# Kernel tuning notes

Hardware: AMD Instinct MI355X
Metric: run time of the kernel (lower is better)

Reference implementation:

```python
import jax, jax.numpy as jnp
import numpy as np

EPS = 1e-08


def _norm(H, add):
    # Faithful to GTN.norm: transpose, mask/set diagonal, row-normalize by degree, transpose back.
    # The original O(N^3) mm(deg_inv_diag, H) is expressed as an O(N^2) row scaling (same math).
    Ht = H.T
    n = Ht.shape[0]
    eye = jnp.eye(n, dtype=H.dtype)
    Ht = Ht * (1.0 - eye)
    if add:
        Ht = Ht + eye
    deg = jnp.sum(Ht, axis=1)
    deg_inv = jnp.where(deg == 0, 0.0, 1.0 / (deg + EPS))
    return (deg_inv[:, None] * Ht).T


def _gtconv(A, w):
    # A: [E, N, N]; w: [C, E, 1, 1] -> softmax over E, weighted sum of adjacency channels.
    s = jax.nn.softmax(w[:, :, 0, 0], axis=1)  # [C, E]
    return jnp.einsum('ce,eij->cij', s, A)     # [C, N, N]


def setup_inputs() -> dict:
    key = jax.random.key(0)
    k = jax.random.split(key, 6)
    E, N, C, w_in, w_out = 5, 2048, 2, 256, 64
    A = jax.random.uniform(k[0], (E, N, N), dtype=jnp.float32)
    X = jax.random.normal(k[1], (N, w_in), dtype=jnp.float32)
    conv_w_l0_1 = jax.random.normal(k[2], (C, E, 1, 1), dtype=jnp.float32)
    conv_w_l0_2 = jax.random.normal(k[3], (C, E, 1, 1), dtype=jnp.float32)
    conv_w_l1 = jax.random.normal(k[4], (C, E, 1, 1), dtype=jnp.float32)
    gcn_weight = jax.random.normal(k[5], (w_in, w_out), dtype=jnp.float32) * (1.0 / np.sqrt(w_in))
    return {"A": A, "X": X, "conv_w_l0_1": conv_w_l0_1, "conv_w_l0_2": conv_w_l0_2,
            "conv_w_l1": conv_w_l1, "gcn_weight": gcn_weight}


def reference(A, X, conv_w_l0_1, conv_w_l0_2, conv_w_l1, gcn_weight):
    N = A.shape[1]
    # Layer 0 (first=True): two GTConvs, meta-path composition via bmm.
    a = _gtconv(A, conv_w_l0_1)            # [C, N, N]
    b = _gtconv(A, conv_w_l0_2)            # [C, N, N]
    H = jnp.einsum('cij,cjk->cik', a, b)   # [C, N, N]
    # Layer 1 (first=False): normalize per channel, then compose with new conv.
    H = jax.vmap(lambda h: _norm(h, False))(H)
    a1 = _gtconv(A, conv_w_l1)
    H = jnp.einsum('cij,cjk->cik', H, a1)
    # GCN readout per channel: mm(norm_add(H_c).T, X @ W), relu, concat along features.
    Xw = X @ gcn_weight                     # [N, w_out]
    Hn = jax.vmap(lambda h: _norm(h, True))(H)   # [C, N, N]
    Xc = jax.nn.relu(jnp.einsum('cji,jk->cik', Hn, Xw))  # [C, N, w_out]
    X_ = jnp.transpose(Xc, (1, 0, 2)).reshape(N, -1)     # [N, C*w_out]
    return X_
```

## Files before the change

### kernel.cpp

```cpp
#include <hip/hip_runtime.h>
#include <cstdint>
#include <cstddef>

typedef unsigned short u16;
typedef __attribute__((ext_vector_type(8))) short short8;
typedef __attribute__((ext_vector_type(4))) float v4f;

static constexpr size_t NN = (size_t)2048 * 2048;
#define N2 2048

typedef __attribute__((address_space(1))) const unsigned int guint;
typedef __attribute__((address_space(3))) unsigned int luint;

__device__ __forceinline__ float b2f_bits(uint32_t hi) { union { uint32_t u; float f; } v; v.u = hi; return v.f; }
__device__ __forceinline__ float b2f(u16 x) { return b2f_bits((uint32_t)x << 16); }
__device__ __forceinline__ u16 f2b(float f) {
  union { float f; uint32_t u; } v; v.f = f;
  uint32_t r = v.u + 0x7fffu + ((v.u >> 16) & 1u);
  return (u16)(r >> 16);
}
__device__ __forceinline__ uint4 pack8(const float* f) {
  uint4 u;
  u.x = (uint32_t)f2b(f[0]) | ((uint32_t)f2b(f[1]) << 16);
  u.y = (uint32_t)f2b(f[2]) | ((uint32_t)f2b(f[3]) << 16);
  u.z = (uint32_t)f2b(f[4]) | ((uint32_t)f2b(f[5]) << 16);
  u.w = (uint32_t)f2b(f[6]) | ((uint32_t)f2b(f[7]) << 16);
  return u;
}
__device__ __forceinline__ void unp8(uint4 u, float* f) {
  f[0] = b2f_bits(u.x << 16); f[1] = b2f_bits(u.x & 0xffff0000u);
  f[2] = b2f_bits(u.y << 16); f[3] = b2f_bits(u.y & 0xffff0000u);
  f[4] = b2f_bits(u.z << 16); f[5] = b2f_bits(u.z & 0xffff0000u);
  f[6] = b2f_bits(u.w << 16); f[7] = b2f_bits(u.w & 0xffff0000u);
}

__global__ __launch_bounds__(256, 2) void conv_kernel(
    const float* __restrict__ A, const float* __restrict__ w1,
    const float* __restrict__ w2, const float* __restrict__ w3,
    const float* __restrict__ X, const float* __restrict__ W,
    u16* __restrict__ abf, u16* __restrict__ bbt, u16* __restrict__ a1t,
    u16* __restrict__ a1r, u16* __restrict__ Xwt)
{
  __shared__ u16 LT[4][64][72];
  const int t = threadIdx.x;
  const int i0 = blockIdx.y * 64, j0 = blockIdx.x * 64;

  const int row = t >> 2;
  const int cq = (t & 3) * 16;

  float fa[5][16];
  #pragma unroll
  for (int e = 0; e < 5; ++e) {
    const float* base = A + (size_t)e * NN + (size_t)(i0 + row) * N2 + (j0 + cq);
    #pragma unroll
    for (int m = 0; m < 4; ++m) {
      float4 v = *(const float4*)(base + m * 4);
      fa[e][m * 4 + 0] = v.x; fa[e][m * 4 + 1] = v.y;
      fa[e][m * 4 + 2] = v.z; fa[e][m * 4 + 3] = v.w;
    }
  }

  const float* wsrc[3] = { w1, w2, w3 };
  #pragma unroll
  for (int c = 0; c < 2; ++c) {
    float sc[3][5];
    #pragma unroll
    for (int q = 0; q < 3; ++q) {
      float v[5], mx = -1e30f, sum = 0.f;
      #pragma unroll
      for (int e = 0; e < 5; ++e) { v[e] = wsrc[q][c * 5 + e]; mx = fmaxf(mx, v[e]); }
      #pragma unroll
      for (int e = 0; e < 5; ++e) { v[e] = expf(v[e] - mx); sum += v[e]; }
      #pragma unroll
      for (int e = 0; e < 5; ++e) sc[q][e] = v[e] / sum;
    }
    float av[16], bv[16], cv[16];
    #pragma unroll
    for (int u = 0; u < 16; ++u) { av[u] = 0.f; bv[u] = 0.f; cv[u] = 0.f; }
    #pragma unroll
    for (int e = 0; e < 5; ++e)
      #pragma unroll
      for (int u = 0; u < 16; ++u) {
        av[u] += sc[0][e] * fa[e][u];
        bv[u] += sc[1][e] * fa[e][u];
        cv[u] += sc[2][e] * fa[e][u];
      }
    {
      uint4* pa = (uint4*)(abf + (size_t)c * NN + (size_t)(i0 + row) * N2 + (j0 + cq));
      pa[0] = pack8(av); pa[1] = pack8(av + 8);
      uint4* pr = (uint4*)(a1r + (size_t)c * NN + (size_t)(i0 + row) * N2 + (j0 + cq));
      pr[0] = pack8(cv); pr[1] = pack8(cv + 8);
    }
    #pragma unroll
    for (int u = 0; u < 16; ++u) {
      LT[c][cq + u][row]     = f2b(bv[u]);
      LT[2 + c][cq + u][row] = f2b(cv[u]);
    }
  }
  __syncthreads();
  {
    const int on = t >> 2;
    const int om = (t & 3) * 16;
    #pragma unroll
    for (int c = 0; c < 2; ++c) {
      const uint4* pb = (const uint4*)&LT[c][on][om];
      uint4* pd = (uint4*)(bbt + (size_t)c * NN + (size_t)(j0 + on) * N2 + (i0 + om));
      pd[0] = pb[0]; pd[1] = pb[1];
      const uint4* pc = (const uint4*)&LT[2 + c][on][om];
      uint4* pe = (uint4*)(a1t + (size_t)c * NN + (size_t)(j0 + on) * N2 + (i0 + om));
      pe[0] = pc[0]; pe[1] = pc[1];
    }
  }
  if (blockIdx.y < 16) {
    const int n = (int)(blockIdx.y * 32 + blockIdx.x) * 4 + (t >> 6);
    const int k = t & 63;
    float acc = 0.f;
    for (int m = 0; m < 256; ++m)
      acc += X[n * 256 + m] * W[m * 64 + k];
    Xwt[(size_t)k * N2 + n] = f2b(acc);
  }
}

template<bool TOUT>
__global__ __launch_bounds__(256, 3) void gemm_kernel(
    const u16* __restrict__ Ain, const u16* __restrict__ Btin,
    u16* __restrict__ Cout, float* __restrict__ csp, float* __restrict__ diag)
{
  const int c = blockIdx.z;
  const u16* Ac = Ain + (size_t)c * NN;
  const u16* Bc = Btin + (size_t)c * NN;
  const int m0 = blockIdx.y * 128, n0 = blockIdx.x * 128;
  const int t = threadIdx.x, w = t >> 6, lane = t & 63;
  const int quad = lane >> 4, r = lane & 15;
  __shared__ u16 SM[128 * 64 + 128 * 64];
  u16* As = SM;
  u16* Bs = SM + 128 * 64;

  v4f zero4 = { 0.f, 0.f, 0.f, 0.f };
  v4f acc[2][8];
  #pragma unroll
  for (int i = 0; i < 2; ++i)
    #pragma unroll
    for (int j = 0; j < 8; ++j) acc[i][j] = zero4;

  const int srow = lane >> 3;
  const int sgran = (lane & 7) ^ srow;

  for (int kt = 0; kt < 2048; kt += 64) {
    __syncthreads();
    #pragma unroll
    for (int i = 0; i < 4; ++i) {
      const int chunk = i * 4 + w;
      const u16* ga = Ac + (size_t)(m0 + chunk * 8 + srow) * N2 + kt + sgran * 8;
      __builtin_amdgcn_global_load_lds((guint*)ga, (luint*)(As + chunk * 512), 16, 0, 0);
    }
    #pragma unroll
    for (int i = 0; i < 4; ++i) {
      const int chunk = i * 4 + w;
      const u16* gb = Bc + (size_t)(n0 + chunk * 8 + srow) * N2 + kt + sgran * 8;
      __builtin_amdgcn_global_load_lds((guint*)gb, (luint*)(Bs + chunk * 512), 16, 0, 0);
    }
    __syncthreads();
    #pragma unroll
    for (int ks = 0; ks < 2; ++ks) {
      const int sl = ((ks * 4 + quad) ^ (r & 7)) * 8;
      short8 af[2], bf[8];
      #pragma unroll
      for (int i = 0; i < 2; ++i)
        af[i] = *(const short8*)(As + (w * 32 + i * 16 + r) * 64 + sl);
      #pragma unroll
      for (int j = 0; j < 8; ++j)
        bf[j] = *(const short8*)(Bs + (j * 16 + r) * 64 + sl);
      #pragma unroll
      for (int i = 0; i < 2; ++i)
        #pragma unroll
        for (int j = 0; j < 8; ++j)
          acc[i][j] = __builtin_amdgcn_mfma_f32_16x16x32_bf16(af[i], bf[j], acc[i][j], 0, 0, 0);
    }
  }
  if (blockIdx.x == blockIdx.y) {
    #pragma unroll
    for (int i = 0; i < 2; ++i) {
      const int rowg = m0 + w * 32 + i * 16 + quad * 4;
      #pragma unroll
      for (int j = 0; j < 8; ++j) {
        const int colg = n0 + j * 16 + r;
        #pragma unroll
        for (int g = 0; g < 4; ++g)
          if (rowg + g == colg) diag[c * N2 + colg] = acc[i][j][g];
      }
    }
  }
  if constexpr (!TOUT) {
    u16* Cc = Cout + (size_t)c * NN;
    #pragma unroll
    for (int i = 0; i < 2; ++i) {
      const int rowg = m0 + w * 32 + i * 16 + quad * 4;
      #pragma unroll
      for (int j = 0; j < 8; ++j) {
        const int colg = n0 + j * 16 + r;
        #pragma unroll
        for (int g = 0; g < 4; ++g)
          Cc[(size_t)(rowg + g) * N2 + colg] = f2b(acc[i][j][g]);
      }
    }
  }
  float s[8];
  #pragma unroll
  for (int j = 0; j < 8; ++j) {
    s[j] = 0.f;
    #pragma unroll
    for (int i = 0; i < 2; ++i)
      #pragma unroll
      for (int g = 0; g < 4; ++g) s[j] += acc[i][j][g];
    s[j] += __shfl_xor(s[j], 16);
    s[j] += __shfl_xor(s[j], 32);
  }
  __syncthreads();
  float* csl = (float*)SM;
  if (quad == 0) {
    #pragma unroll
    for (int j = 0; j < 8; ++j) csl[w * 128 + j * 16 + r] = s[j];
  }
  __syncthreads();
  if (t < 128) {
    const float v = csl[t] + csl[128 + t] + csl[256 + t] + csl[384 + t];
    csp[((size_t)(c * 16) + blockIdx.y) * N2 + n0 + t] = v;
  }
  if constexpr (TOUT) {
    u16* tb = SM;
    u16* Cc = Cout + (size_t)c * NN;
    #pragma unroll
    for (int h = 0; h < 2; ++h) {
      __syncthreads();
      #pragma unroll
      for (int i = 0; i < 2; ++i) {
        #pragma unroll
        for (int jl = 0; jl < 4; ++jl) {
          const int j = h * 4 + jl;
          #pragma unroll
          for (int g = 0; g < 4; ++g)
            tb[(jl * 16 + r) * 136 + (w * 32 + i * 16 + quad * 4 + g)] = f2b(acc[i][j][g]);
        }
      }
      __syncthreads();
      const int rown = t >> 2, seg = t & 3;
      const u16* ps = tb + rown * 136 + seg * 32;
      uint4* pd = (uint4*)(Cc + (size_t)(n0 + h * 64 + rown) * N2 + m0 + seg * 32);
      pd[0] = ((const uint4*)ps)[0];
      pd[1] = ((const uint4*)ps)[1];
      pd[2] = ((const uint4*)ps)[2];
      pd[3] = ((const uint4*)ps)[3];
    }
  }
}

__global__ __launch_bounds__(256) void zgemm_kernel(
    const u16* __restrict__ Ht, const u16* __restrict__ Xwt, float* __restrict__ Zp,
    const float* __restrict__ csp, const float* __restrict__ diag,
    float* __restrict__ ci, float* __restrict__ wv)
{
  const int c = blockIdx.z, split = blockIdx.y;
  const int m0 = blockIdx.x * 128;
  const u16* Ac = Ht + (size_t)c * NN;
  const int t = threadIdx.x, w = t >> 6, lane = t & 63;
  const int quad = lane >> 4, r = lane & 15;
  __shared__ u16 As[128 * 64];
  __shared__ u16 Bs[64 * 64];

  v4f zero4 = { 0.f, 0.f, 0.f, 0.f };
  v4f acc[2][4];
  #pragma unroll
  for (int i = 0; i < 2; ++i)
    #pragma unroll
    for (int j = 0; j < 4; ++j) acc[i][j] = zero4;

  const int srow = lane >> 3;
  const int sgran = (lane & 7) ^ srow;

  for (int kk = 0; kk < 2; ++kk) {
    const int kt = split * 128 + kk * 64;
    __syncthreads();
    #pragma unroll
    for (int i = 0; i < 4; ++i) {
      const int chunk = i * 4 + w;
      const u16* ga = Ac + (size_t)(m0 + chunk * 8 + srow) * N2 + kt + sgran * 8;
      __builtin_amdgcn_global_load_lds((guint*)ga, (luint*)(As + chunk * 512), 16, 0, 0);
    }
    #pragma unroll
    for (int i = 0; i < 2; ++i) {
      const int chunk = i * 4 + w;
      const u16* gb = Xwt + (size_t)(chunk * 8 + srow) * N2 + kt + sgran * 8;
      __builtin_amdgcn_global_load_lds((guint*)gb, (luint*)(Bs + chunk * 512), 16, 0, 0);
    }
    __syncthreads();
    #pragma unroll
    for (int ks = 0; ks < 2; ++ks) {
      const int sl = ((ks * 4 + quad) ^ (r & 7)) * 8;
      short8 af[2], bf[4];
      #pragma unroll
      for (int i = 0; i < 2; ++i)
        af[i] = *(const short8*)(As + (w * 32 + i * 16 + r) * 64 + sl);
      #pragma unroll
      for (int j = 0; j < 4; ++j)
        bf[j] = *(const short8*)(Bs + (j * 16 + r) * 64 + sl);
      #pragma unroll
      for (int i = 0; i < 2; ++i)
        #pragma unroll
        for (int j = 0; j < 4; ++j)
          acc[i][j] = __builtin_amdgcn_mfma_f32_16x16x32_bf16(af[i], bf[j], acc[i][j], 0, 0, 0);
    }
  }
  const size_t pbase = (size_t)(split * 2 + c) * 64;
  #pragma unroll
  for (int i = 0; i < 2; ++i) {
    const int rowg = m0 + w * 32 + i * 16 + quad * 4;
    #pragma unroll
    for (int j = 0; j < 4; ++j) {
      const int colg = j * 16 + r;
      *(v4f*)(Zp + (pbase + colg) * (size_t)N2 + rowg) = acc[i][j];
    }
  }
  if (blockIdx.x == 0 && blockIdx.y == 0) {
    for (int q = t; q < 2048; q += 256) {
      float cs = 0.f;
      #pragma unroll
      for (int s = 0; s < 16; ++s) cs += csp[((size_t)(c * 16) + s) * N2 + q];
      const float deg = cs - diag[c * N2 + q];
      const float v = (deg == 0.f) ? 0.f : 1.f / (deg + 1e-8f);
      ci[c * N2 + q] = v;
      wv[c * N2 + q] = v * deg;
    }
  }
}

__global__ __launch_bounds__(256) void dcol_kernel(
    const u16* __restrict__ Ht, const u16* __restrict__ a1r,
    const float* __restrict__ ci, const float* __restrict__ wv,
    float* __restrict__ dp, float* __restrict__ cp)
{
  const int qg = blockIdx.x, c = blockIdx.y;
  const int p0 = threadIdx.x * 8;
  float dacc[8] = {0,0,0,0,0,0,0,0};
  float cacc[8] = {0,0,0,0,0,0,0,0};
  const u16* hb = Ht  + (size_t)c * NN + (size_t)(qg * 16) * N2 + p0;
  const u16* ab = a1r + (size_t)c * NN + (size_t)(qg * 16) * N2 + p0;
  for (int qq = 0; qq < 16; ++qq) {
    const int q = qg * 16 + qq;
    const float cq = ci[c * N2 + q];
    const float wq = wv[c * N2 + q];
    uint4 hu = *(const uint4*)(hb + (size_t)qq * N2);
    uint4 au = *(const uint4*)(ab + (size_t)qq * N2);
    float h[8], a[8];
    unp8(hu, h); unp8(au, a);
    #pragma unroll
    for (int u = 0; u < 8; ++u) {
      cacc[u] += wq * a[u];
      const float tv = cq * h[u] * a[u];
      dacc[u] += (p0 + u == q) ? 0.f : tv;
    }
  }
  float* dd = dp + (size_t)(c * 128 + qg) * N2 + p0;
  float* cd = cp + (size_t)(c * 128 + qg) * N2 + p0;
  v4f d0 = { dacc[0], dacc[1], dacc[2], dacc[3] };
  v4f d1 = { dacc[4], dacc[5], dacc[6], dacc[7] };
  v4f c0 = { cacc[0], cacc[1], cacc[2], cacc[3] };
  v4f c1 = { cacc[4], cacc[5], cacc[6], cacc[7] };
  *(v4f*)dd = d0; *(v4f*)(dd + 4) = d1;
  *(v4f*)cd = c0; *(v4f*)(cd + 4) = c1;
}

__global__ __launch_bounds__(256) void yfix_kernel(
    const float* __restrict__ Zp, const float* __restrict__ ci,
    const float* __restrict__ diag1, const u16* __restrict__ Xwt,
    u16* __restrict__ Yt)
{
  const int idx = blockIdx.x * 256 + threadIdx.x;
  const int i = idx & 2047, k = (idx >> 11) & 63, c = idx >> 17;
  float z = 0.f;
  #pragma unroll
  for (int s = 0; s < 16; ++s)
    z += Zp[(size_t)((s * 2 + c) * 64 + k) * N2 + i];
  const float xw = b2f(Xwt[(size_t)k * N2 + i]);
  const float y = ci[c * N2 + i] * (z - diag1[c * N2 + i] * xw);
  Yt[(size_t)c * 64 * N2 + (size_t)k * N2 + i] = f2b(y);
}

__global__ void fin_kernel(const float* __restrict__ dp, const float* __restrict__ cp,
                           float* __restrict__ diag2, float* __restrict__ dinv2)
{
  const int idx = blockIdx.x * 256 + threadIdx.x;
  const int c = idx >> 11, i = idx & 2047;
  float ds = 0.f, cs = 0.f;
  for (int b = 0; b < 128; ++b) {
    ds += dp[(size_t)(c * 128 + b) * N2 + i];
    cs += cp[(size_t)(c * 128 + b) * N2 + i];
  }
  const float deg = cs - ds + 1.0f;
  diag2[idx] = ds;
  dinv2[idx] = (deg == 0.f) ? 0.f : 1.f / (deg + 1e-8f);
}

__global__ __launch_bounds__(256) void tgemm_kernel(
    const u16* __restrict__ a1t, const u16* __restrict__ Yt, float* __restrict__ Tp)
{
  const int c = blockIdx.z, split = blockIdx.y;
  const int m0 = blockIdx.x * 128;
  const u16* Ac = a1t + (size_t)c * NN;
  const u16* Bc = Yt + (size_t)c * (64 * (size_t)N2);
  const int t = threadIdx.x, w = t >> 6, lane = t & 63;
  const int quad = lane >> 4, r = lane & 15;
  __shared__ u16 As[128 * 64];
  __shared__ u16 Bs[64 * 64];

  v4f zero4 = { 0.f, 0.f, 0.f, 0.f };
  v4f acc[2][4];
  #pragma unroll
  for (int i = 0; i < 2; ++i)
    #pragma unroll
    for (int j = 0; j < 4; ++j) acc[i][j] = zero4;

  const int srow = lane >> 3;
  const int sgran = (lane & 7) ^ srow;

  for (int kk = 0; kk < 2; ++kk) {
    const int kt = split * 128 + kk * 64;
    __syncthreads();
    #pragma unroll
    for (int i = 0; i < 4; ++i) {
      const int chunk = i * 4 + w;
      const u16* ga = Ac + (size_t)(m0 + chunk * 8 + srow) * N2 + kt + sgran * 8;
      __builtin_amdgcn_global_load_lds((guint*)ga, (luint*)(As + chunk * 512), 16, 0, 0);
    }
    #pragma unroll
    for (int i = 0; i < 2; ++i) {
      const int chunk = i * 4 + w;
      const u16* gb = Bc + (size_t)(chunk * 8 + srow) * N2 + kt + sgran * 8;
      __builtin_amdgcn_global_load_lds((guint*)gb, (luint*)(Bs + chunk * 512), 16, 0, 0);
    }
    __syncthreads();
    #pragma unroll
    for (int ks = 0; ks < 2; ++ks) {
      const int sl = ((ks * 4 + quad) ^ (r & 7)) * 8;
      short8 af[2], bf[4];
      #pragma unroll
      for (int i = 0; i < 2; ++i)
        af[i] = *(const short8*)(As + (w * 32 + i * 16 + r) * 64 + sl);
      #pragma unroll
      for (int j = 0; j < 4; ++j)
        bf[j] = *(const short8*)(Bs + (j * 16 + r) * 64 + sl);
      #pragma unroll
      for (int i = 0; i < 2; ++i)
        #pragma unroll
        for (int j = 0; j < 4; ++j)
          acc[i][j] = __builtin_amdgcn_mfma_f32_16x16x32_bf16(af[i], bf[j], acc[i][j], 0, 0, 0);
    }
  }
  const size_t pbase = (size_t)(split * 2 + c) * 2048;
  #pragma unroll
  for (int i = 0; i < 2; ++i) {
    const int rowg = m0 + w * 32 + i * 16 + quad * 4;
    #pragma unroll
    for (int j = 0; j < 4; ++j) {
      const int colg = j * 16 + r;
      #pragma unroll
      for (int g = 0; g < 4; ++g)
        Tp[(pbase + rowg + g) * 64 + colg] = acc[i][j][g];
    }
  }
}

__global__ void epilogue_kernel(const float* __restrict__ Tp, const float* __restrict__ diag2,
                                const float* __restrict__ dinv2, const u16* __restrict__ Xwt,
                                float* __restrict__ out)
{
  const int idx = blockIdx.x * 256 + threadIdx.x;
  const int k = idx & 63;
  const int c = (idx >> 6) & 1;
  const int i = idx >> 7;
  float T = 0.f;
  #pragma unroll
  for (int s = 0; s < 16; ++s)
    T += Tp[((size_t)(s * 2 + c) * 2048 + i) * 64 + k];
  const float hd = diag2[c * N2 + i];
  const float dv = dinv2[c * N2 + i];
  const float xw = b2f(Xwt[(size_t)k * N2 + i]);
  float v = dv * (T - hd * xw + xw);
  v = v > 0.f ? v : 0.f;
  out[(size_t)i * 128 + c * 64 + k] = v;
}

extern "C" void kernel_launch(void* const* d_in, const int* in_sizes, int n_in,
                              void* d_out, int out_size, void* d_ws, size_t ws_size,
                              hipStream_t stream) {
  const float* A  = (const float*)d_in[0];
  const float* X  = (const float*)d_in[1];
  const float* w1 = (const float*)d_in[2];
  const float* w2 = (const float*)d_in[3];
  const float* w3 = (const float*)d_in[4];
  const float* W  = (const float*)d_in[5];
  float* out = (float*)d_out;
  char* ws = (char*)d_ws;

  u16*   abf   = (u16*)(ws + 0);
  u16*   bbt   = (u16*)(ws + 16777216);
  u16*   a1t   = (u16*)(ws + 33554432);
  u16*   a1r   = (u16*)(ws + 50331648);
  u16*   Ht    = (u16*)(ws + 67108864);
  u16*   Xwt   = (u16*)(ws + 83886080);
  float* cspa  = (float*)(ws + 84148224);
  float* diag1 = (float*)(ws + 84410368);
  float* ci1   = (float*)(ws + 84426752);
  float* w2v   = (float*)(ws + 84443136);
  float* diag2 = (float*)(ws + 84459520);
  float* dinv2 = (float*)(ws + 84475904);
  float* Zp    = (float*)(ws + 0);
  float* dp    = (float*)(ws + 16777216);
  float* cp    = (float*)(ws + 18874368);
  u16*   Yt    = (u16*)(ws + 20971520);
  float* Tp    = (float*)(ws + 50331648);

  conv_kernel<<<dim3(32, 32), 256, 0, stream>>>(A, w1, w2, w3, X, W, abf, bbt, a1t, a1r, Xwt);
  gemm_kernel<true><<<dim3(16, 16, 2), 256, 0, stream>>>(abf, bbt, Ht, cspa, diag1);
  zgemm_kernel<<<dim3(16, 16, 2), 256, 0, stream>>>(Ht, Xwt, Zp, cspa, diag1, ci1, w2v);
  dcol_kernel<<<dim3(128, 2), 256, 0, stream>>>(Ht, a1r, ci1, w2v, dp, cp);
  yfix_kernel<<<1024, 256, 0, stream>>>(Zp, ci1, diag1, Xwt, Yt);
  fin_kernel<<<16, 256, 0, stream>>>(dp, cp, diag2, dinv2);
  tgemm_kernel<<<dim3(16, 16, 2), 256, 0, stream>>>(a1t, Yt, Tp);
  epilogue_kernel<<<1024, 256, 0, stream>>>(Tp, diag2, dinv2, Xwt, out);
}
```

Measured before the change: 264.9 us.

## Rework conv kernel thread mapping and halve split-K in skinny GEMMs

The conv kernel now uses 512 threads, each handling 8 columns for both channels. Softmax weights are hoisted once into scalar registers, the transpose LDS tile uses an XOR swizzle instead of padding, and the Xw computation is spread over fewer blocks. The zgemm and tgemm skinny GEMMs move from 16 to 8 K-splits with 256-wide K per block, and the yfix and epilogue reductions shrink to match. This is meant to cut register pressure and LDS bank conflicts in the conv kernel and to reduce partial-sum traffic and reduction work. The cost is fewer blocks in parallel for the skinny GEMMs.

```diff
diff --git a/kernel.cpp b/kernel.cpp
--- a/kernel.cpp
+++ b/kernel.cpp
@@ -33,90 +33,97 @@
   f[4] = b2f_bits(u.z << 16); f[5] = b2f_bits(u.z & 0xffff0000u);
   f[6] = b2f_bits(u.w << 16); f[7] = b2f_bits(u.w & 0xffff0000u);
 }
-
-__global__ __launch_bounds__(256, 2) void conv_kernel(
+__device__ __forceinline__ float sgprf(float x) {
+  union { float f; int i; } v; v.f = x;
+  v.i = __builtin_amdgcn_readfirstlane(v.i);
+  return v.f;
+}
+
+__global__ __launch_bounds__(512, 2) void conv_kernel(
     const float* __restrict__ A, const float* __restrict__ w1,
     const float* __restrict__ w2, const float* __restrict__ w3,
     const float* __restrict__ X, const float* __restrict__ W,
     u16* __restrict__ abf, u16* __restrict__ bbt, u16* __restrict__ a1t,
     u16* __restrict__ a1r, u16* __restrict__ Xwt)
 {
-  __shared__ u16 LT[4][64][72];
+  __shared__ u16 LT[4][64 * 64];
   const int t = threadIdx.x;
   const int i0 = blockIdx.y * 64, j0 = blockIdx.x * 64;
-
-  const int row = t >> 2;
-  const int cq = (t & 3) * 16;
-
-  float fa[5][16];
+  const int m = t >> 3;
+  const int cg = t & 7;
+  const int n0 = cg * 8;
+
+  float sc[3][2][5];
+  {
+    const float* wsrc[3] = { w1, w2, w3 };
+    for (int q = 0; q < 3; ++q)
+      for (int c = 0; c < 2; ++c) {
+        float v[5], mx = -1e30f, sum = 0.f;
+        #pragma unroll
+        for (int e = 0; e < 5; ++e) { v[e] = wsrc[q][c * 5 + e]; mx = fmaxf(mx, v[e]); }
+        #pragma unroll
+        for (int e = 0; e < 5; ++e) { v[e] = expf(v[e] - mx); sum += v[e]; }
+        #pragma unroll
+        for (int e = 0; e < 5; ++e) sc[q][c][e] = sgprf(v[e] / sum);
+      }
+  }
+
+  float av[2][8], bv[2][8], cv[2][8];
+  #pragma unroll
+  for (int c = 0; c < 2; ++c)
+    #pragma unroll
+    for (int u = 0; u < 8; ++u) { av[c][u] = 0.f; bv[c][u] = 0.f; cv[c][u] = 0.f; }
+
   #pragma unroll
   for (int e = 0; e < 5; ++e) {
-    const float* base = A + (size_t)e * NN + (size_t)(i0 + row) * N2 + (j0 + cq);
-    #pragma unroll
-    for (int m = 0; m < 4; ++m) {
-      float4 v = *(const float4*)(base + m * 4);
-      fa[e][m * 4 + 0] = v.x; fa[e][m * 4 + 1] = v.y;
-      fa[e][m * 4 + 2] = v.z; fa[e][m * 4 + 3] = v.w;
-    }
-  }
-
-  const float* wsrc[3] = { w1, w2, w3 };
+    const float* base = A + (size_t)e * NN + (size_t)(i0 + m) * N2 + (j0 + n0);
+    float4 x0 = ((const float4*)base)[0];
+    float4 x1 = ((const float4*)base)[1];
+    float f[8] = { x0.x, x0.y, x0.z, x0.w, x1.x, x1.y, x1.z, x1.w };
+    #pragma unroll
+    for (int c = 0; c < 2; ++c)
+      #pragma unroll
+      for (int u = 0; u < 8; ++u) {
+        av[c][u] += sc[0][c][e] * f[u];
+        bv[c][u] += sc[1][c][e] * f[u];
+        cv[c][u] += sc[2][c][e] * f[u];
+      }
+  }
+
   #pragma unroll
   for (int c = 0; c < 2; ++c) {
-    float sc[3][5];
-    #pragma unroll
-    for (int q = 0; q < 3; ++q) {
-      float v[5], mx = -1e30f, sum = 0.f;
-      #pragma unroll
-      for (int e = 0; e < 5; ++e) { v[e] = wsrc[q][c * 5 + e]; mx = fmaxf(mx, v[e]); }
-      #pragma unroll
-      for (int e = 0; e < 5; ++e) { v[e] = expf(v[e] - mx); sum += v[e]; }
-      #pragma unroll
-      for (int e = 0; e < 5; ++e) sc[q][e] = v[e] / sum;
-    }
-    float av[16], bv[16], cv[16];
-    #pragma unroll
-    for (int u = 0; u < 16; ++u) { av[u] = 0.f; bv[u] = 0.f; cv[u] = 0.f; }
-    #pragma unroll
-    for (int e = 0; e < 5; ++e)
-      #pragma unroll
-      for (int u = 0; u < 16; ++u) {
-        av[u] += sc[0][e] * fa[e][u];
-        bv[u] += sc[1][e] * fa[e][u];
-        cv[u] += sc[2][e] * fa[e][u];
-      }
-    {
-      uint4* pa = (uint4*)(abf + (size_t)c * NN + (size_t)(i0 + row) * N2 + (j0 + cq));
-      pa[0] = pack8(av); pa[1] = pack8(av + 8);
-      uint4* pr = (uint4*)(a1r + (size_t)c * NN + (size_t)(i0 + row) * N2 + (j0 + cq));
-      pr[0] = pack8(cv); pr[1] = pack8(cv + 8);
-    }
-    #pragma unroll
-    for (int u = 0; u < 16; ++u) {
-      LT[c][cq + u][row]     = f2b(bv[u]);
-      LT[2 + c][cq + u][row] = f2b(cv[u]);
-    }
-  }
+    *(uint4*)(abf + (size_t)c * NN + (size_t)(i0 + m) * N2 + (j0 + n0)) = pack8(av[c]);
+    *(uint4*)(a1r + (size_t)c * NN + (size_t)(i0 + m) * N2 + (j0 + n0)) = pack8(cv[c]);
+  }
+  const int swb = ((m >> 3) ^ cg) & 7;
+  const int mlo = m & 7;
+  #pragma unroll
+  for (int c = 0; c < 2; ++c)
+    #pragma unroll
+    for (int u = 0; u < 8; ++u) {
+      const int idx = (n0 + u) * 64 + swb * 8 + mlo;
+      LT[c][idx]     = f2b(bv[c][u]);
+      LT[2 + c][idx] = f2b(cv[c][u]);
+    }
   __syncthreads();
   {
-    const int on = t >> 2;
-    const int om = (t & 3) * 16;
+    const int on = t >> 3;
+    const int mb = t & 7;
+    const int src = on * 64 + (((mb ^ (on >> 3)) & 7) * 8);
     #pragma unroll
     for (int c = 0; c < 2; ++c) {
-      const uint4* pb = (const uint4*)&LT[c][on][om];
-      uint4* pd = (uint4*)(bbt + (size_t)c * NN + (size_t)(j0 + on) * N2 + (i0 + om));
-      pd[0] = pb[0]; pd[1] = pb[1];
-      const uint4* pc = (const uint4*)&LT[2 + c][on][om];
-      uint4* pe = (uint4*)(a1t + (size_t)c * NN + (size_t)(j0 + on) * N2 + (i0 + om));
-      pe[0] = pc[0]; pe[1] = pc[1];
-    }
-  }
-  if (blockIdx.y < 16) {
-    const int n = (int)(blockIdx.y * 32 + blockIdx.x) * 4 + (t >> 6);
+      *(uint4*)(bbt + (size_t)c * NN + (size_t)(j0 + on) * N2 + (i0 + mb * 8)) =
+          *(const uint4*)&LT[c][src];
+      *(uint4*)(a1t + (size_t)c * NN + (size_t)(j0 + on) * N2 + (i0 + mb * 8)) =
+          *(const uint4*)&LT[2 + c][src];
+    }
+  }
+  if (blockIdx.y < 8) {
+    const int n = (int)(blockIdx.y * 32 + blockIdx.x) * 8 + (t >> 6);
     const int k = t & 63;
     float acc = 0.f;
-    for (int m = 0; m < 256; ++m)
-      acc += X[n * 256 + m] * W[m * 64 + k];
+    for (int mm = 0; mm < 256; ++mm)
+      acc += X[n * 256 + mm] * W[mm * 64 + k];
     Xwt[(size_t)k * N2 + n] = f2b(acc);
   }
 }
@@ -278,8 +285,8 @@
   const int srow = lane >> 3;
   const int sgran = (lane & 7) ^ srow;
 
-  for (int kk = 0; kk < 2; ++kk) {
-    const int kt = split * 128 + kk * 64;
+  for (int kk = 0; kk < 4; ++kk) {
+    const int kt = split * 256 + kk * 64;
     __syncthreads();
     #pragma unroll
     for (int i = 0; i < 4; ++i) {
@@ -379,7 +386,7 @@
   const int i = idx & 2047, k = (idx >> 11) & 63, c = idx >> 17;
   float z = 0.f;
   #pragma unroll
-  for (int s = 0; s < 16; ++s)
+  for (int s = 0; s < 8; ++s)
     z += Zp[(size_t)((s * 2 + c) * 64 + k) * N2 + i];
   const float xw = b2f(Xwt[(size_t)k * N2 + i]);
   const float y = ci[c * N2 + i] * (z - diag1[c * N2 + i] * xw);
@@ -423,8 +430,8 @@
   const int srow = lane >> 3;
   const int sgran = (lane & 7) ^ srow;
 
-  for (int kk = 0; kk < 2; ++kk) {
-    const int kt = split * 128 + kk * 64;
+  for (int kk = 0; kk < 4; ++kk) {
+    const int kt = split * 256 + kk * 64;
     __syncthreads();
     #pragma unroll
     for (int i = 0; i < 4; ++i) {
@@ -480,7 +487,7 @@
   const int i = idx >> 7;
   float T = 0.f;
   #pragma unroll
-  for (int s = 0; s < 16; ++s)
+  for (int s = 0; s < 8; ++s)
     T += Tp[((size_t)(s * 2 + c) * 2048 + i) * 64 + k];
   const float hd = diag2[c * N2 + i];
   const float dv = dinv2[c * N2 + i];
@@ -520,12 +527,12 @@
   u16*   Yt    = (u16*)(ws + 20971520);
   float* Tp    = (float*)(ws + 50331648);
 
-  conv_kernel<<<dim3(32, 32), 256, 0, stream>>>(A, w1, w2, w3, X, W, abf, bbt, a1t, a1r, Xwt);
+  conv_kernel<<<dim3(32, 32), 512, 0, stream>>>(A, w1, w2, w3, X, W, abf, bbt, a1t, a1r, Xwt);
   gemm_kernel<true><<<dim3(16, 16, 2), 256, 0, stream>>>(abf, bbt, Ht, cspa, diag1);
-  zgemm_kernel<<<dim3(16, 16, 2), 256, 0, stream>>>(Ht, Xwt, Zp, cspa, diag1, ci1, w2v);
+  zgemm_kernel<<<dim3(16, 8, 2), 256, 0, stream>>>(Ht, Xwt, Zp, cspa, diag1, ci1, w2v);
   dcol_kernel<<<dim3(128, 2), 256, 0, stream>>>(Ht, a1r, ci1, w2v, dp, cp);
   yfix_kernel<<<1024, 256, 0, stream>>>(Zp, ci1, diag1, Xwt, Yt);
   fin_kernel<<<16, 256, 0, stream>>>(dp, cp, diag2, dinv2);
-  tgemm_kernel<<<dim3(16, 16, 2), 256, 0, stream>>>(a1t, Yt, Tp);
+  tgemm_kernel<<<dim3(16, 8, 2), 256, 0, stream>>>(a1t, Yt, Tp);
   epilogue_kernel<<<1024, 256, 0, stream>>>(Tp, diag2, dinv2, Xwt, out);
 }
```

Measured after the change: 246.4 us. -7.0%, faster.
